# Performance work log

Measured on AMD Instinct MI355X. Metric: run time of the kernel, lower is better.

## Reference

```python
import jax, jax.numpy as jnp
import numpy as np

L_X, L_D = 10, 4
T_N, T_F = 0.0, 1.0
C_BG = (1.0, 1.0, 1.0)


def _pe(p, L):
    # NeRF positional encoding: [sin(2^i pi p), cos(2^i pi p)] for i in 0..L-1
    freqs = (2.0 ** jnp.arange(L, dtype=p.dtype)) * jnp.pi  # [L]
    ang = p[..., None, :] * freqs[:, None]  # [..., L, 3]
    enc = jnp.concatenate([jnp.sin(ang), jnp.cos(ang)], axis=-1)  # [..., L, 6]
    return enc.reshape(p.shape[:-1] + (6 * L,))


def setup_inputs() -> dict:
    key = jax.random.key(0)
    ks = jax.random.split(key, 16)
    B, N, H, HL = 2048, 128, 256, 128
    Dx, Dd = 6 * L_X, 6 * L_D  # 60, 24
    o = jax.random.normal(ks[0], (B, 3), dtype=jnp.float32) * 0.5
    d = jax.random.normal(ks[1], (B, 3), dtype=jnp.float32)
    d = d / jnp.linalg.norm(d, axis=-1, keepdims=True)
    # stratified coarse samples in [t_n, t_f] (sorted by construction)
    u = jax.random.uniform(ks[2], (B, N), dtype=jnp.float32)
    t = T_N + (T_F - T_N) * ((jnp.arange(N, dtype=jnp.float32) / N)[None, :] + u / N)
    w = lambda k, fi, fo: jax.random.normal(k, (fi, fo), dtype=jnp.float32) * jnp.sqrt(2.0 / fi)
    Wh = jax.random.normal(ks[4], (4, H, H), dtype=jnp.float32) * jnp.sqrt(2.0 / H)
    return dict(
        o=o, d=d, t=t,
        W0=w(ks[3], Dx, H), b0=jnp.zeros((H,), jnp.float32),
        Wh=Wh, bh=jnp.zeros((4, H), jnp.float32),
        W5=w(ks[5], H + Dx, H), b5=jnp.zeros((H,), jnp.float32),
        W6=w(ks[6], H, H), b6=jnp.zeros((H,), jnp.float32),
        W7=w(ks[7], H, H), b7=jnp.zeros((H,), jnp.float32),
        Ws=w(ks[8], H, 1), bs=jnp.zeros((1,), jnp.float32),
        Wf=w(ks[9], H, H), bf=jnp.zeros((H,), jnp.float32),
        Wm=w(ks[10], H + Dd, HL), bm=jnp.zeros((HL,), jnp.float32),
        Wr=w(ks[11], HL, 3), br=jnp.zeros((3,), jnp.float32),
    )


def _forward(o, d, t, W0, b0, Wh, bh, W5, b5, W6, b6, W7, b7, Ws, bs, Wf, bf, Wm, bm, Wr, br):
    B, N = t.shape
    # sample points along rays: x = o + t * d  -> [B, N, 3]
    x = o[:, None, :] + t[..., None] * d[:, None, :]
    px = _pe(x, L_X).reshape(B * N, -1)            # [BN, 60]
    pd = _pe(d, L_D)                               # [B, 24]
    pd = jnp.broadcast_to(pd[:, None, :], (B, N, pd.shape[-1])).reshape(B * N, -1)
    # radiance field MLP (standard NeRF trunk with skip at layer 5)
    h = jax.nn.relu(px @ W0 + b0)
    for i in range(4):
        h = jax.nn.relu(h @ Wh[i] + bh[i])
    h = jnp.concatenate([h, px], axis=-1)
    h = jax.nn.relu(h @ W5 + b5)
    h = jax.nn.relu(h @ W6 + b6)
    h = jax.nn.relu(h @ W7 + b7)
    sigma = jax.nn.relu(h @ Ws + bs).reshape(B, N)  # density
    feat = h @ Wf + bf
    h2 = jax.nn.relu(jnp.concatenate([feat, pd], axis=-1) @ Wm + bm)
    rgb = jax.nn.sigmoid(h2 @ Wr + br).reshape(B, N, 3)
    # volume rendering weights (matches torch pad/exp/cumsum logic)
    delta = jnp.concatenate([t[:, 1:] - t[:, :-1], jnp.full((B, 1), 1e8, t.dtype)], axis=1)
    mass = sigma * delta                             # [B, N]
    mass0 = jnp.concatenate([jnp.zeros((B, 1), t.dtype), mass], axis=1)
    alpha = 1.0 - jnp.exp(-mass0[:, 1:])
    T = jnp.exp(-jnp.cumsum(mass0[:, :-1], axis=1))
    wgt = T * alpha                                  # [B, N]
    C = jnp.sum(wgt[..., None] * rgb, axis=1)        # [B, 3]
    bg = jnp.asarray(C_BG, dtype=C.dtype)[None, :]
    C = C + (1.0 - jnp.sum(wgt, axis=1, keepdims=True)) * bg
    return C


def reference(o, d, t, W0, b0, Wh, bh, W5, b5, W6, b6, W7, b7, Ws, bs, Wf, bf, Wm, bm, Wr, br):
    return _forward(o, d, t, W0, b0, Wh, bh, W5, b5, W6, b6, W7, b7, Ws, bs, Wf, bf, Wm, bm, Wr, br)
```

## Files before the change

### kernel.cpp

```cpp
#include <hip/hip_runtime.h>
#include <hip/hip_fp16.h>
#include <math.h>

typedef __bf16   bf16x8 __attribute__((ext_vector_type(8)));
typedef _Float16 f16x8  __attribute__((ext_vector_type(8)));
typedef float    f32x4  __attribute__((ext_vector_type(4)));

#define AH  264
#define TOT 589824

#define OFF_W0T   0
#define OFF_WHT   16384
#define OFF_W5AT  278528
#define OFF_W5BT  344064
#define OFF_W6T   360448
#define OFF_W7T   425984
#define OFF_WFT   491520
#define OFF_WMAT  557056

__global__ void prep_weights(const float* __restrict__ W0, const float* __restrict__ Wh,
                             const float* __restrict__ W5, const float* __restrict__ W6,
                             const float* __restrict__ W7, const float* __restrict__ Wf,
                             const float* __restrict__ Wm, __bf16* __restrict__ ws) {
  int idx = blockIdx.x * blockDim.x + threadIdx.x;
  if (idx >= TOT) return;
  float v = 0.f;
  if (idx < OFF_WHT)        { int j = idx;            int n=j>>6, k=j&63;   v = (k<60)? W0[k*256+n] : 0.f; }
  else if (idx < OFF_W5AT)  { int j = idx - OFF_WHT;  int i=j>>16, r=j&65535, n=r>>8, k=r&255; v = Wh[i*65536+k*256+n]; }
  else if (idx < OFF_W5BT)  { int j = idx - OFF_W5AT; int n=j>>8, k=j&255;  v = W5[k*256+n]; }
  else if (idx < OFF_W6T)   { int j = idx - OFF_W5BT; int n=j>>6, k=j&63;   v = (k<60)? W5[(256+k)*256+n] : 0.f; }
  else if (idx < OFF_W7T)   { int j = idx - OFF_W6T;  int n=j>>8, k=j&255;  v = W6[k*256+n]; }
  else if (idx < OFF_WFT)   { int j = idx - OFF_W7T;  int n=j>>8, k=j&255;  v = W7[k*256+n]; }
  else if (idx < OFF_WMAT)  { int j = idx - OFF_WFT;  int n=j>>8, k=j&255;  v = Wf[k*256+n]; }
  else                      { int j = idx - OFF_WMAT; int n=j>>8, k=j&255;  v = Wm[k*128+n]; }
  __bf16 hi = (__bf16)v;
  ws[idx] = hi;
  ws[TOT + idx] = (__bf16)(v - (float)hi);
}

#define MFMA16(A,B,C) __builtin_amdgcn_mfma_f32_16x16x32_bf16((A),(B),(C),0,0,0)

template<int NT, int HALF>
__device__ __forceinline__ void mfma_layer(__bf16* aHi, __bf16* aLo, const __half* pxh,
    const __bf16* __restrict__ wHi, const __bf16* __restrict__ wLo, int kStr, int nkc,
    const __bf16* __restrict__ xHi, const __bf16* __restrict__ xLo,
    const float* __restrict__ bias, const float* __restrict__ pdW,
    bool relu, int tid) {
  const int wave = tid >> 6, lane = tid & 63;
  const int lm = lane & 15, kq = lane >> 4;
  const int mBase = HALF ? 0 : (wave >> 2) * 64;
  const int nBase = (HALF ? wave : (wave & 3)) * (NT * 16);
  f32x4 acc[4][NT];
#pragma unroll
  for (int mt = 0; mt < 4; ++mt)
#pragma unroll
    for (int nt = 0; nt < NT; ++nt)
#pragma unroll
      for (int e = 0; e < 4; ++e) acc[mt][nt][e] = 0.f;

  if (nkc >= 2) {
    if constexpr (NT <= 2) {
      const int kb0 = kq * 8;
      int wr[NT];
#pragma unroll
      for (int nt = 0; nt < NT; ++nt) wr[nt] = (nBase + nt*16 + lm)*kStr + kb0;
      const int ab = (mBase + lm)*AH + kb0;
      bf16x8 bhA[NT], blA[NT], bhB[NT], blB[NT];
#pragma unroll
      for (int nt = 0; nt < NT; ++nt) {
        bhA[nt] = *(const bf16x8*)(wHi + wr[nt]);
        blA[nt] = *(const bf16x8*)(wLo + wr[nt]);
      }
      for (int kc = 0; kc < nkc; kc += 2) {
#pragma unroll
        for (int nt = 0; nt < NT; ++nt) {
          bhB[nt] = *(const bf16x8*)(wHi + wr[nt] + (kc+1)*32);
          blB[nt] = *(const bf16x8*)(wLo + wr[nt] + (kc+1)*32);
        }
#pragma unroll
        for (int mp = 0; mp < 2; ++mp) {
          const int r0 = ab + mp*32*AH + kc*32;
          bf16x8 a0h = *(const bf16x8*)(aHi + r0);
          bf16x8 a0l = *(const bf16x8*)(aLo + r0);
          bf16x8 a1h = *(const bf16x8*)(aHi + r0 + 16*AH);
          bf16x8 a1l = *(const bf16x8*)(aLo + r0 + 16*AH);
#pragma unroll
          for (int nt = 0; nt < NT; ++nt) {
            acc[2*mp  ][nt] = MFMA16(a0h, bhA[nt], acc[2*mp  ][nt]);
            acc[2*mp+1][nt] = MFMA16(a1h, bhA[nt], acc[2*mp+1][nt]);
            acc[2*mp  ][nt] = MFMA16(a0h, blA[nt], acc[2*mp  ][nt]);
            acc[2*mp+1][nt] = MFMA16(a1h, blA[nt], acc[2*mp+1][nt]);
            acc[2*mp  ][nt] = MFMA16(a0l, bhA[nt], acc[2*mp  ][nt]);
            acc[2*mp+1][nt] = MFMA16(a1l, bhA[nt], acc[2*mp+1][nt]);
          }
        }
        if (kc + 2 < nkc) {
#pragma unroll
          for (int nt = 0; nt < NT; ++nt) {
            bhA[nt] = *(const bf16x8*)(wHi + wr[nt] + (kc+2)*32);
            blA[nt] = *(const bf16x8*)(wLo + wr[nt] + (kc+2)*32);
          }
        }
#pragma unroll
        for (int mp = 0; mp < 2; ++mp) {
          const int r0 = ab + mp*32*AH + (kc+1)*32;
          bf16x8 a0h = *(const bf16x8*)(aHi + r0);
          bf16x8 a0l = *(const bf16x8*)(aLo + r0);
          bf16x8 a1h = *(const bf16x8*)(aHi + r0 + 16*AH);
          bf16x8 a1l = *(const bf16x8*)(aLo + r0 + 16*AH);
#pragma unroll
          for (int nt = 0; nt < NT; ++nt) {
            acc[2*mp  ][nt] = MFMA16(a0h, bhB[nt], acc[2*mp  ][nt]);
            acc[2*mp+1][nt] = MFMA16(a1h, bhB[nt], acc[2*mp+1][nt]);
            acc[2*mp  ][nt] = MFMA16(a0h, blB[nt], acc[2*mp  ][nt]);
            acc[2*mp+1][nt] = MFMA16(a1h, blB[nt], acc[2*mp+1][nt]);
            acc[2*mp  ][nt] = MFMA16(a0l, bhB[nt], acc[2*mp  ][nt]);
            acc[2*mp+1][nt] = MFMA16(a1l, bhB[nt], acc[2*mp+1][nt]);
          }
        }
      }
    } else {
      for (int kc = 0; kc < nkc; ++kc) {
        const int kb = kc*32 + kq*8;
        bf16x8 ah[4], al[4], bh[NT], bl[NT];
#pragma unroll
        for (int mt = 0; mt < 4; ++mt) {
          const int off = (mBase + mt*16 + lm)*AH + kb;
          ah[mt] = *(const bf16x8*)(aHi + off);
          al[mt] = *(const bf16x8*)(aLo + off);
        }
#pragma unroll
        for (int nt = 0; nt < NT; ++nt) {
          const int ro = (nBase + nt*16 + lm)*kStr + kb;
          bh[nt] = *(const bf16x8*)(wHi + ro);
          bl[nt] = *(const bf16x8*)(wLo + ro);
        }
#pragma unroll
        for (int p = 0; p < 3; ++p)
#pragma unroll
          for (int mt = 0; mt < 4; ++mt)
#pragma unroll
            for (int nt = 0; nt < NT; ++nt)
              acc[mt][nt] = __builtin_amdgcn_mfma_f32_16x16x32_bf16(
                  (p == 2) ? al[mt] : ah[mt],
                  (p == 1) ? bl[nt] : bh[nt],
                  acc[mt][nt], 0, 0, 0);
      }
    }
  }
  if (xHi) {
#pragma unroll
    for (int kc = 0; kc < 2; ++kc) {
      const int kb = kc*32 + kq*8;
      bf16x8 bh[NT], bl[NT];
#pragma unroll
      for (int nt = 0; nt < NT; ++nt) {
        const int ro = (nBase + nt*16 + lm)*64 + kb;
        bh[nt] = *(const bf16x8*)(xHi + ro);
        bl[nt] = *(const bf16x8*)(xLo + ro);
      }
#pragma unroll
      for (int mp = 0; mp < 2; ++mp) {
        bf16x8 ah[2], al[2];
#pragma unroll
        for (int i = 0; i < 2; ++i) {
          const f16x8 pv = *(const f16x8*)((const _Float16*)pxh + (mBase + (2*mp+i)*16 + lm)*64 + kb);
#pragma unroll
          for (int j = 0; j < 8; ++j) {
            float v = (float)pv[j];
            __bf16 h = (__bf16)v;
            ah[i][j] = h;
            al[i][j] = (__bf16)(v - (float)h);
          }
        }
#pragma unroll
        for (int nt = 0; nt < NT; ++nt) {
          acc[2*mp  ][nt] = MFMA16(ah[0], bh[nt], acc[2*mp  ][nt]);
          acc[2*mp+1][nt] = MFMA16(ah[1], bh[nt], acc[2*mp+1][nt]);
          acc[2*mp  ][nt] = MFMA16(ah[0], bl[nt], acc[2*mp  ][nt]);
          acc[2*mp+1][nt] = MFMA16(ah[1], bl[nt], acc[2*mp+1][nt]);
          acc[2*mp  ][nt] = MFMA16(al[0], bh[nt], acc[2*mp  ][nt]);
          acc[2*mp+1][nt] = MFMA16(al[1], bh[nt], acc[2*mp+1][nt]);
        }
      }
    }
  }
  __syncthreads();
#pragma unroll
  for (int mt = 0; mt < 4; ++mt)
#pragma unroll
    for (int nt = 0; nt < NT; ++nt) {
      const int col = nBase + nt*16 + lm;
      float bv = bias[col] + (pdW ? pdW[col] : 0.f);
#pragma unroll
      for (int r = 0; r < 4; ++r) {
        const int row = mBase + mt*16 + kq*4 + r;
        float v = acc[mt][nt][r] + bv;
        if (relu) v = fmaxf(v, 0.f);
        __bf16 h = (__bf16)v;
        aHi[row*AH + col] = h;
        aLo[row*AH + col] = (__bf16)(v - (float)h);
      }
    }
  __syncthreads();
}

template<int HALF>
__global__ __launch_bounds__(512, 4)
void nerf_main(
    const float* __restrict__ ro, const float* __restrict__ rd, const float* __restrict__ tin,
    const float* __restrict__ b0, const float* __restrict__ bh,
    const float* __restrict__ b5, const float* __restrict__ b6,
    const float* __restrict__ b7,
    const float* __restrict__ Wsig, const float* __restrict__ bs,
    const float* __restrict__ bfb,
    const float* __restrict__ Wm, const float* __restrict__ bm,
    const float* __restrict__ Wr, const float* __restrict__ br,
    const __bf16* __restrict__ wsHi, const __bf16* __restrict__ wsLo,
    float* __restrict__ part, float* __restrict__ out) {
  constexpr int M = HALF ? 64 : 128;
  __shared__ __align__(16) __bf16 aHi[M * AH];
  __shared__ __align__(16) __bf16 aLo[M * AH];
  __shared__ __align__(16) unsigned char pxred[M * 128];
  __shared__ __align__(16) float  pdBuf[24];
  __shared__ __align__(16) float  pdW[128];
  __shared__ __align__(16) float  tBuf[M + 4];
  __shared__ __align__(16) float  sigBuf[M];
  __shared__ __align__(16) float  rgbBuf[M * 3];

  __half* pxh = (__half*)pxred;
  float*  red = (float*)pxred;

  const int blk  = blockIdx.x;
  const int ray  = HALF ? (blk >> 1) : blk;
  const int S    = HALF ? (blk & 1) * 64 : 0;
  const int tid  = threadIdx.x;

  if (tid < M) {
    const int m = tid;
    float tv = tin[ray*128 + S + m];
    tBuf[m] = tv;
    float xs[3];
#pragma unroll
    for (int c = 0; c < 3; ++c) xs[c] = ro[ray*3 + c] + tv * rd[ray*3 + c];
#pragma unroll
    for (int i = 0; i < 10; ++i)
#pragma unroll
      for (int c = 0; c < 3; ++c) {
        float a = ldexpf(xs[c], i);
        pxh[m*64 + i*6 + c]     = __float2half(sinpif(a));
        pxh[m*64 + i*6 + 3 + c] = __float2half(cospif(a));
      }
#pragma unroll
    for (int j = 60; j < 64; ++j) pxh[m*64 + j] = __float2half(0.f);
  } else if (tid < M + 24) {
    int j = tid - M;
    int i = j / 6, r = j % 6;
    float a = ldexpf(rd[ray*3 + (r % 3)], i);
    pdBuf[j] = (r < 3) ? sinpif(a) : cospif(a);
  } else if (tid == M + 24) {
    tBuf[M] = (S + M < 128) ? tin[ray*128 + S + M] : 0.f;
  }
  __syncthreads();
  if (tid >= 256 && tid < 384) {
    int c = tid - 256;
    float s = 0.f;
#pragma unroll
    for (int j = 0; j < 24; ++j) s += pdBuf[j] * Wm[(256 + j)*128 + c];
    pdW[c] = s;
  }
  __syncthreads();

  constexpr int NTF = HALF ? 2 : 4;
  constexpr int NTW = HALF ? 1 : 2;

  mfma_layer<NTF, HALF>(aHi, aLo, pxh, nullptr, nullptr, 0, 0,
                        wsHi + OFF_W0T, wsLo + OFF_W0T, b0, nullptr, true, tid);
  for (int i = 0; i < 4; ++i)
    mfma_layer<NTF, HALF>(aHi, aLo, pxh, wsHi + OFF_WHT + i*65536, wsLo + OFF_WHT + i*65536, 256, 8,
                          nullptr, nullptr, bh + i*256, nullptr, true, tid);
  mfma_layer<NTF, HALF>(aHi, aLo, pxh, wsHi + OFF_W5AT, wsLo + OFF_W5AT, 256, 8,
                        wsHi + OFF_W5BT, wsLo + OFF_W5BT, b5, nullptr, true, tid);
  mfma_layer<NTF, HALF>(aHi, aLo, pxh, wsHi + OFF_W6T, wsLo + OFF_W6T, 256, 8,
                        nullptr, nullptr, b6, nullptr, true, tid);
  mfma_layer<NTF, HALF>(aHi, aLo, pxh, wsHi + OFF_W7T, wsLo + OFF_W7T, 256, 8,
                        nullptr, nullptr, b7, nullptr, true, tid);

  {
    constexpr int TPS = 512 / M;
    const int m = tid / TPS, q = tid % TPS;
    const int kn = 256 / TPS;
    float s = 0.f;
    for (int k8 = q*kn; k8 < q*kn + kn; k8 += 8) {
      bf16x8 vh = *(const bf16x8*)(aHi + m*AH + k8);
      bf16x8 vl = *(const bf16x8*)(aLo + m*AH + k8);
#pragma unroll
      for (int j = 0; j < 8; ++j) s += ((float)vh[j] + (float)vl[j]) * Wsig[k8 + j];
    }
    red[tid] = s;
    __syncthreads();
    if (tid < M) {
      float sm = bs[0];
#pragma unroll
      for (int j = 0; j < TPS; ++j) sm += red[TPS*tid + j];
      sigBuf[tid] = fmaxf(sm, 0.f);
    }
    __syncthreads();
  }

  mfma_layer<NTF, HALF>(aHi, aLo, nullptr, wsHi + OFF_WFT, wsLo + OFF_WFT, 256, 8,
                        nullptr, nullptr, bfb, nullptr, false, tid);

  mfma_layer<NTW, HALF>(aHi, aLo, nullptr, wsHi + OFF_WMAT, wsLo + OFF_WMAT, 256, 8,
                        nullptr, nullptr, bm, pdW, true, tid);

  {
    constexpr int TPS = 512 / M;
    const int m = tid / TPS, q = tid % TPS;
    const int kn = 128 / TPS;
    float r0s = 0.f, r1s = 0.f, r2s = 0.f;
    for (int k8 = q*kn; k8 < q*kn + kn; k8 += 8) {
      bf16x8 vh = *(const bf16x8*)(aHi + m*AH + k8);
      bf16x8 vl = *(const bf16x8*)(aLo + m*AH + k8);
#pragma unroll
      for (int j = 0; j < 8; ++j) {
        float hv = (float)vh[j] + (float)vl[j];
        r0s += hv * Wr[(k8 + j)*3 + 0];
        r1s += hv * Wr[(k8 + j)*3 + 1];
        r2s += hv * Wr[(k8 + j)*3 + 2];
      }
    }
    red[tid] = r0s; red[512 + tid] = r1s; red[1024 + tid] = r2s;
    __syncthreads();
    if (tid < M) {
#pragma unroll
      for (int c = 0; c < 3; ++c) {
        float sm = br[c];
#pragma unroll
        for (int j = 0; j < TPS; ++j) sm += red[c*512 + TPS*tid + j];
        rgbBuf[tid*3 + c] = 1.f / (1.f + expf(-sm));
      }
    }
    __syncthreads();
  }

  if (tid == 0) {
    float T = 1.f, c0 = 0.f, c1 = 0.f, c2 = 0.f, wsum = 0.f;
    for (int m = 0; m < M; ++m) {
      float delta = (S + m < 127) ? (tBuf[m + 1] - tBuf[m]) : 1e8f;
      float e = expf(-sigBuf[m] * delta);
      float w = T * (1.f - e);
      c0 += w * rgbBuf[m*3 + 0];
      c1 += w * rgbBuf[m*3 + 1];
      c2 += w * rgbBuf[m*3 + 2];
      wsum += w;
      T *= e;
    }
    if (HALF) {
      float* p = part + blk*5;
      p[0] = c0; p[1] = c1; p[2] = c2; p[3] = wsum; p[4] = T;
    } else {
      float bg = 1.f - wsum;
      out[ray*3 + 0] = c0 + bg;
      out[ray*3 + 1] = c1 + bg;
      out[ray*3 + 2] = c2 + bg;
    }
  }
}

__global__ void combine(const float* __restrict__ part, float* __restrict__ out) {
  int r = blockIdx.x * blockDim.x + threadIdx.x;
  if (r >= 2048) return;
  const float* p0 = part + (2*r)*5;
  const float* p1 = p0 + 5;
  float T0 = p0[4];
  float wsum = p0[3] + T0 * p1[3];
  float bg = 1.f - wsum;
#pragma unroll
  for (int c = 0; c < 3; ++c)
    out[r*3 + c] = p0[c] + T0 * p1[c] + bg;
}

extern "C" void kernel_launch(void* const* d_in, const int* in_sizes, int n_in,
                              void* d_out, int out_size, void* d_ws, size_t ws_size,
                              hipStream_t stream) {
  const float* ro  = (const float*)d_in[0];
  const float* rd  = (const float*)d_in[1];
  const float* t   = (const float*)d_in[2];
  const float* W0  = (const float*)d_in[3];
  const float* b0  = (const float*)d_in[4];
  const float* Wh  = (const float*)d_in[5];
  const float* bh  = (const float*)d_in[6];
  const float* W5  = (const float*)d_in[7];
  const float* b5  = (const float*)d_in[8];
  const float* W6  = (const float*)d_in[9];
  const float* b6  = (const float*)d_in[10];
  const float* W7  = (const float*)d_in[11];
  const float* b7  = (const float*)d_in[12];
  const float* Wsg = (const float*)d_in[13];
  const float* bs  = (const float*)d_in[14];
  const float* Wf  = (const float*)d_in[15];
  const float* bfb = (const float*)d_in[16];
  const float* Wm  = (const float*)d_in[17];
  const float* bm  = (const float*)d_in[18];
  const float* Wr  = (const float*)d_in[19];
  const float* br  = (const float*)d_in[20];
  float* out = (float*)d_out;

  __bf16* wsHi = (__bf16*)d_ws;
  __bf16* wsLo = wsHi + TOT;
  float*  part = (float*)((char*)d_ws + (size_t)2 * TOT * 2);

  const size_t needSplit = (size_t)2 * TOT * 2 + (size_t)4096 * 5 * 4;

  prep_weights<<<(TOT + 255)/256, 256, 0, stream>>>(W0, Wh, W5, W6, W7, Wf, Wm, wsHi);
  if (ws_size >= needSplit) {
    nerf_main<1><<<4096, 512, 0, stream>>>(ro, rd, t, b0, bh, b5, b6, b7,
                                           Wsg, bs, bfb, Wm, bm, Wr, br,
                                           wsHi, wsLo, part, out);
    combine<<<8, 256, 0, stream>>>(part, out);
  } else {
    nerf_main<0><<<2048, 512, 0, stream>>>(ro, rd, t, b0, bh, b5, b6, b7,
                                           Wsg, bs, bfb, Wm, bm, Wr, br,
                                           wsHi, wsLo, part, out);
  }
}
```

Before: 1.271 ms.

## Software-pipeline A-fragment LDS loads and pack hi/lo epilogue stores via lane shuffles

Restructures the NT<=2 GEMM inner loop so the activation fragments for the next M-half are loaded from LDS while the current half's MFMAs issue, using double-buffered register sets. The epilogue now exchanges bf16 hi/lo halves between adjacent lanes with a shuffle, so each lane writes one 32-bit word instead of two 16-bit stores. The hi and lo activation buffers are merged into one shared array with a 16-element offset, likely to shift LDS bank mapping between them. This adds register pressure and a cross-lane shuffle per element, and issues one redundant wrap-around prefetch on the last iteration.

```diff
diff --git a/kernel.cpp b/kernel.cpp
--- a/kernel.cpp
+++ b/kernel.cpp
@@ -71,28 +71,45 @@
         bhA[nt] = *(const bf16x8*)(wHi + wr[nt]);
         blA[nt] = *(const bf16x8*)(wLo + wr[nt]);
       }
+      bf16x8 x0h, x0l, x1h, x1l, y0h, y0l, y1h, y1l;
+      {
+        const int r0 = ab;
+        x0h = *(const bf16x8*)(aHi + r0);
+        x0l = *(const bf16x8*)(aLo + r0);
+        x1h = *(const bf16x8*)(aHi + r0 + 16*AH);
+        x1l = *(const bf16x8*)(aLo + r0 + 16*AH);
+      }
+#define MFMA_STEP(A0H,A0L,A1H,A1L,BH,BL,E0,E1)                         \
+      _Pragma("unroll")                                                \
+      for (int nt = 0; nt < NT; ++nt) {                                \
+        acc[E0][nt] = MFMA16(A0H, BH[nt], acc[E0][nt]);                \
+        acc[E1][nt] = MFMA16(A1H, BH[nt], acc[E1][nt]);                \
+        acc[E0][nt] = MFMA16(A0H, BL[nt], acc[E0][nt]);                \
+        acc[E1][nt] = MFMA16(A1H, BL[nt], acc[E1][nt]);                \
+        acc[E0][nt] = MFMA16(A0L, BH[nt], acc[E0][nt]);                \
+        acc[E1][nt] = MFMA16(A1L, BH[nt], acc[E1][nt]);                \
+      }
       for (int kc = 0; kc < nkc; kc += 2) {
 #pragma unroll
         for (int nt = 0; nt < NT; ++nt) {
           bhB[nt] = *(const bf16x8*)(wHi + wr[nt] + (kc+1)*32);
           blB[nt] = *(const bf16x8*)(wLo + wr[nt] + (kc+1)*32);
         }
-#pragma unroll
-        for (int mp = 0; mp < 2; ++mp) {
-          const int r0 = ab + mp*32*AH + kc*32;
-          bf16x8 a0h = *(const bf16x8*)(aHi + r0);
-          bf16x8 a0l = *(const bf16x8*)(aLo + r0);
-          bf16x8 a1h = *(const bf16x8*)(aHi + r0 + 16*AH);
-          bf16x8 a1l = *(const bf16x8*)(aLo + r0 + 16*AH);
-#pragma unroll
-          for (int nt = 0; nt < NT; ++nt) {
-            acc[2*mp  ][nt] = MFMA16(a0h, bhA[nt], acc[2*mp  ][nt]);
-            acc[2*mp+1][nt] = MFMA16(a1h, bhA[nt], acc[2*mp+1][nt]);
-            acc[2*mp  ][nt] = MFMA16(a0h, blA[nt], acc[2*mp  ][nt]);
-            acc[2*mp+1][nt] = MFMA16(a1h, blA[nt], acc[2*mp+1][nt]);
-            acc[2*mp  ][nt] = MFMA16(a0l, bhA[nt], acc[2*mp  ][nt]);
-            acc[2*mp+1][nt] = MFMA16(a1l, bhA[nt], acc[2*mp+1][nt]);
-          }
+        {
+          const int r0 = ab + 32*AH + kc*32;
+          y0h = *(const bf16x8*)(aHi + r0);
+          y0l = *(const bf16x8*)(aLo + r0);
+          y1h = *(const bf16x8*)(aHi + r0 + 16*AH);
+          y1l = *(const bf16x8*)(aLo + r0 + 16*AH);
+          MFMA_STEP(x0h, x0l, x1h, x1l, bhA, blA, 0, 1)
+        }
+        {
+          const int r0 = ab + (kc+1)*32;
+          x0h = *(const bf16x8*)(aHi + r0);
+          x0l = *(const bf16x8*)(aLo + r0);
+          x1h = *(const bf16x8*)(aHi + r0 + 16*AH);
+          x1l = *(const bf16x8*)(aLo + r0 + 16*AH);
+          MFMA_STEP(y0h, y0l, y1h, y1l, bhA, blA, 2, 3)
         }
         if (kc + 2 < nkc) {
 #pragma unroll
@@ -101,24 +118,25 @@
             blA[nt] = *(const bf16x8*)(wLo + wr[nt] + (kc+2)*32);
           }
         }
-#pragma unroll
-        for (int mp = 0; mp < 2; ++mp) {
-          const int r0 = ab + mp*32*AH + (kc+1)*32;
-          bf16x8 a0h = *(const bf16x8*)(aHi + r0);
-          bf16x8 a0l = *(const bf16x8*)(aLo + r0);
-          bf16x8 a1h = *(const bf16x8*)(aHi + r0 + 16*AH);
-          bf16x8 a1l = *(const bf16x8*)(aLo + r0 + 16*AH);
-#pragma unroll
-          for (int nt = 0; nt < NT; ++nt) {
-            acc[2*mp  ][nt] = MFMA16(a0h, bhB[nt], acc[2*mp  ][nt]);
-            acc[2*mp+1][nt] = MFMA16(a1h, bhB[nt], acc[2*mp+1][nt]);
-            acc[2*mp  ][nt] = MFMA16(a0h, blB[nt], acc[2*mp  ][nt]);
-            acc[2*mp+1][nt] = MFMA16(a1h, blB[nt], acc[2*mp+1][nt]);
-            acc[2*mp  ][nt] = MFMA16(a0l, bhB[nt], acc[2*mp  ][nt]);
-            acc[2*mp+1][nt] = MFMA16(a1l, bhB[nt], acc[2*mp+1][nt]);
-          }
-        }
-      }
+        {
+          const int r0 = ab + 32*AH + (kc+1)*32;
+          y0h = *(const bf16x8*)(aHi + r0);
+          y0l = *(const bf16x8*)(aLo + r0);
+          y1h = *(const bf16x8*)(aHi + r0 + 16*AH);
+          y1l = *(const bf16x8*)(aLo + r0 + 16*AH);
+          MFMA_STEP(x0h, x0l, x1h, x1l, bhB, blB, 0, 1)
+        }
+        {
+          const int kc2 = (kc + 2 < nkc) ? kc + 2 : 0;
+          const int r0 = ab + kc2*32;
+          x0h = *(const bf16x8*)(aHi + r0);
+          x0l = *(const bf16x8*)(aLo + r0);
+          x1h = *(const bf16x8*)(aHi + r0 + 16*AH);
+          x1l = *(const bf16x8*)(aLo + r0 + 16*AH);
+          MFMA_STEP(y0h, y0l, y1h, y1l, bhB, blB, 2, 3)
+        }
+      }
+#undef MFMA_STEP
     } else {
       for (int kc = 0; kc < nkc; ++kc) {
         const int kb = kc*32 + kq*8;
@@ -186,11 +204,13 @@
     }
   }
   __syncthreads();
+  const int par = lm & 1;
 #pragma unroll
   for (int mt = 0; mt < 4; ++mt)
 #pragma unroll
     for (int nt = 0; nt < NT; ++nt) {
       const int col = nBase + nt*16 + lm;
+      const int colB = col & ~1;
       float bv = bias[col] + (pdW ? pdW[col] : 0.f);
 #pragma unroll
       for (int r = 0; r < 4; ++r) {
@@ -198,8 +218,14 @@
         float v = acc[mt][nt][r] + bv;
         if (relu) v = fmaxf(v, 0.f);
         __bf16 h = (__bf16)v;
-        aHi[row*AH + col] = h;
-        aLo[row*AH + col] = (__bf16)(v - (float)h);
+        __bf16 l = (__bf16)(v - (float)h);
+        unsigned hu = (unsigned)__builtin_bit_cast(unsigned short, h);
+        unsigned lu = (unsigned)__builtin_bit_cast(unsigned short, l);
+        unsigned send = par ? hu : lu;
+        unsigned recv = (unsigned)__shfl_xor((int)send, 1, 64);
+        unsigned word = par ? ((lu << 16) | (recv & 0xffffu))
+                            : ((recv << 16) | hu);
+        *(unsigned*)((par ? aLo : aHi) + row*AH + colB) = word;
       }
     }
   __syncthreads();
@@ -219,14 +245,16 @@
     const __bf16* __restrict__ wsHi, const __bf16* __restrict__ wsLo,
     float* __restrict__ part, float* __restrict__ out) {
   constexpr int M = HALF ? 64 : 128;
-  __shared__ __align__(16) __bf16 aHi[M * AH];
-  __shared__ __align__(16) __bf16 aLo[M * AH];
+  __shared__ __align__(16) __bf16 actBuf[2*M*AH + 16];
   __shared__ __align__(16) unsigned char pxred[M * 128];
   __shared__ __align__(16) float  pdBuf[24];
   __shared__ __align__(16) float  pdW[128];
   __shared__ __align__(16) float  tBuf[M + 4];
   __shared__ __align__(16) float  sigBuf[M];
   __shared__ __align__(16) float  rgbBuf[M * 3];
+
+  __bf16* aHi = actBuf;
+  __bf16* aLo = actBuf + M*AH + 16;
 
   __half* pxh = (__half*)pxred;
   float*  red = (float*)pxred;
```

After: 1.342 ms. 1.06x slower.
